# Kernel tuning notes

Hardware: AMD Instinct MI355X
Metric: run time of the kernel (lower is better)

Reference implementation:

```python
import jax, jax.numpy as jnp
import numpy as np

N = 100000      # nodes
E = 1600000     # edges
IN = 128        # in_channels
HID = 32        # hidden_channels
HEADS = 4
G = 256         # number of graphs in the batch
NEG_SLOPE = 0.2


def setup_inputs() -> dict:
    key = jax.random.key(0)
    ks = jax.random.split(key, 20)
    s = 0.1
    d = {
        'x': jax.random.normal(ks[0], (N, IN), jnp.float32),
        'edge_index': jax.random.randint(ks[1], (2, E), 0, N, dtype=jnp.int64),
        'batch': jnp.sort(jax.random.randint(ks[2], (N,), 0, G, dtype=jnp.int64)),
        # conv1: IN -> HID per head, HEADS heads, concat
        'W1': jax.random.normal(ks[3], (IN, HEADS * HID), jnp.float32) * s,
        'a_src1': jax.random.normal(ks[4], (HEADS, HID), jnp.float32) * s,
        'a_dst1': jax.random.normal(ks[5], (HEADS, HID), jnp.float32) * s,
        'b1': jnp.zeros((HEADS * HID,), jnp.float32),
        # conv2: HEADS*HID -> HID per head, HEADS heads, concat
        'W2': jax.random.normal(ks[6], (HEADS * HID, HEADS * HID), jnp.float32) * s,
        'a_src2': jax.random.normal(ks[7], (HEADS, HID), jnp.float32) * s,
        'a_dst2': jax.random.normal(ks[8], (HEADS, HID), jnp.float32) * s,
        'b2': jnp.zeros((HEADS * HID,), jnp.float32),
        # conv3: HEADS*HID -> HID, 1 head, no concat (mean over heads is identity)
        'W3': jax.random.normal(ks[9], (HEADS * HID, HID), jnp.float32) * s,
        'a_src3': jax.random.normal(ks[10], (1, HID), jnp.float32) * s,
        'a_dst3': jax.random.normal(ks[11], (1, HID), jnp.float32) * s,
        'b3': jnp.zeros((HID,), jnp.float32),
        # final readout
        'fc_w': jax.random.normal(ks[12], (HID, 1), jnp.float32) * s,
        'fc_b': jnp.zeros((1,), jnp.float32),
    }
    return d


def _gat_layer(x, src, dst, W, a_s, a_d, b, concat):
    """One PyG-style GATConv: edge attention logits, per-destination softmax, scatter-aggregate."""
    n = x.shape[0]
    H, C = a_s.shape
    h = (x @ W).reshape(n, H, C)                       # [N, H, C]
    asrc = (h * a_s).sum(-1)                           # [N, H]
    adst = (h * a_d).sum(-1)                           # [N, H]
    e = jax.nn.leaky_relu(asrc[src] + adst[dst], NEG_SLOPE)   # [Etot, H]
    m = jax.ops.segment_max(e, dst, num_segments=n)    # per-dst max (self-loops guarantee non-empty)
    ex = jnp.exp(e - m[dst])
    den = jax.ops.segment_sum(ex, dst, num_segments=n)
    alpha = ex / (den[dst] + 1e-16)                    # segment softmax, [Etot, H]
    out = jax.ops.segment_sum(alpha[:, :, None] * h[src], dst, num_segments=n)  # [N, H, C]
    if concat:
        return out.reshape(n, H * C) + b
    return out.mean(axis=1) + b


def reference(x, edge_index, batch, W1, a_src1, a_dst1, b1, W2, a_src2, a_dst2, b2,
              W3, a_src3, a_dst3, b3, fc_w, fc_b):
    n = x.shape[0]
    loops = jnp.arange(n, dtype=edge_index.dtype)      # GATConv adds self-loops by default
    src = jnp.concatenate([edge_index[0], loops])
    dst = jnp.concatenate([edge_index[1], loops])

    h = jax.nn.elu(_gat_layer(x, src, dst, W1, a_src1, a_dst1, b1, True))
    h = jax.nn.elu(_gat_layer(h, src, dst, W2, a_src2, a_dst2, b2, True))
    h = jax.nn.elu(_gat_layer(h, src, dst, W3, a_src3, a_dst3, b3, False))

    counts = jax.ops.segment_sum(jnp.ones((n,), h.dtype), batch, num_segments=G)
    pooled = jax.ops.segment_sum(h, batch, num_segments=G) / jnp.maximum(counts, 1.0)[:, None]
    # dropout p=0.5 is identity in eval mode
    return pooled @ fc_w + fc_b                        # [G, 1]
```

## Files before the change

### kernel.cpp

```cpp
#include <hip/hip_runtime.h>
#include <hip/hip_bf16.h>
#include <math.h>

#define NEG_SLOPE 0.2f
#define CHUNK 6144

typedef short bf16x8 __attribute__((ext_vector_type(8)));
typedef float f32x4  __attribute__((ext_vector_type(4)));

__device__ __forceinline__ float leaky(float x){ return x > 0.f ? x : NEG_SLOPE*x; }
__device__ __forceinline__ float elu(float x){ return x > 0.f ? x : expm1f(x); }

__device__ __forceinline__ ushort f2bf(float f){
  uint u = __float_as_uint(f);
  u += 0x7fffu + ((u >> 16) & 1u);
  return (ushort)(u >> 16);
}
__device__ __forceinline__ uint pk2(float lo, float hi){
  return (uint)f2bf(lo) | ((uint)f2bf(hi) << 16);
}
__device__ __forceinline__ float2 bfpair(uint v){
  return make_float2(__uint_as_float(v << 16), __uint_as_float(v & 0xffff0000u));
}

__global__ __launch_bounds__(256) void k_histA(const int* __restrict__ ei, int E,
                                               int* __restrict__ bucketCount){
  __shared__ int hist[512];
  for (int b = threadIdx.x; b < 512; b += 256) hist[b] = 0;
  __syncthreads();
  int base = blockIdx.x * 2048;
  int cnt = min(2048, E - base);
  for (int i = threadIdx.x; i < cnt; i += 256)
    atomicAdd(&hist[ei[E + base + i] >> 8], 1);
  __syncthreads();
  for (int b = threadIdx.x; b < 512; b += 256)
    if (hist[b]) atomicAdd(&bucketCount[b], hist[b]);
}

__global__ __launch_bounds__(256) void k_scanB(const int* __restrict__ bucketCount, int NB,
                        int* __restrict__ bucketBase, int* __restrict__ gcursor, int E){
  __shared__ int s[512];
  for (int b = threadIdx.x; b < 512; b += 256)
    s[b] = (b < NB) ? bucketCount[b] : 0;
  __syncthreads();
  if (threadIdx.x == 0){
    int run = 0;
    for (int b = 0; b < NB; b++){ int v = s[b]; s[b] = run; run += v; }
  }
  __syncthreads();
  for (int b = threadIdx.x; b < NB; b += 256){
    bucketBase[b] = s[b]; gcursor[b] = s[b];
  }
  if (threadIdx.x == 0) bucketBase[NB] = E;
}

__global__ __launch_bounds__(256) void k_scatA(const int* __restrict__ ei, int E, int NB,
                         int* __restrict__ gcursor, uint* __restrict__ tmp){
  __shared__ uint stageS[CHUNK];
  __shared__ uint stageD[CHUNK];
  __shared__ int hist[512], pre[512], cur[512], gbase[512];
  __shared__ int scanArr[256];
  int tid = threadIdx.x;
  int base = blockIdx.x * CHUNK;
  int cnt = min(CHUNK, E - base);
  for (int b = tid; b < 512; b += 256) hist[b] = 0;
  __syncthreads();
  for (int i = tid; i < cnt; i += 256)
    atomicAdd(&hist[ei[E + base + i] >> 8], 1);
  __syncthreads();
  int a0 = hist[2*tid], a1 = hist[2*tid+1];
  scanArr[tid] = a0 + a1;
  __syncthreads();
  for (int st = 1; st < 256; st <<= 1){
    int v = (tid >= st) ? scanArr[tid - st] : 0;
    __syncthreads();
    scanArr[tid] += v;
    __syncthreads();
  }
  int eb = tid ? scanArr[tid-1] : 0;
  pre[2*tid] = eb;        cur[2*tid] = eb;
  pre[2*tid+1] = eb + a0; cur[2*tid+1] = eb + a0;
  if (2*tid < NB && a0 > 0)   gbase[2*tid]   = atomicAdd(&gcursor[2*tid],   a0);
  if (2*tid+1 < NB && a1 > 0) gbase[2*tid+1] = atomicAdd(&gcursor[2*tid+1], a1);
  __syncthreads();
  for (int i = tid; i < cnt; i += 256){
    int s = ei[base + i];
    int d = ei[E + base + i];
    int lpos = atomicAdd(&cur[d >> 8], 1);
    stageS[lpos] = (uint)s; stageD[lpos] = (uint)d;
  }
  __syncthreads();
  for (int i = tid; i < cnt; i += 256){
    uint d = stageD[i];
    int b = d >> 8;
    tmp[gbase[b] + (i - pre[b])] = (stageS[i] << 8) | (d & 255u);
  }
}

__global__ __launch_bounds__(256) void k_csr(const uint* __restrict__ tmp,
                      const int* __restrict__ bucketBase,
                      int N, int NB, int* __restrict__ offsets, int* __restrict__ csr){
  int b = blockIdx.x;
  int nodeBase = b << 8;
  int nNodes = min(256, N - nodeBase);
  int eBeg = bucketBase[b], eEnd = bucketBase[b+1];
  __shared__ int deg[256], cur[256];
  int tid = threadIdx.x;
  deg[tid] = 0;
  __syncthreads();
  for (int e = eBeg + tid; e < eEnd; e += 256)
    atomicAdd(&deg[tmp[e] & 255u], 1);
  __syncthreads();
  cur[tid] = deg[tid];
  __syncthreads();
  for (int st = 1; st < 256; st <<= 1){
    int w = (tid >= st) ? cur[tid - st] : 0;
    __syncthreads();
    cur[tid] += w;
    __syncthreads();
  }
  int excl = tid ? cur[tid-1] : 0;
  __syncthreads();
  cur[tid] = excl;
  if (tid < nNodes) offsets[nodeBase + tid] = eBeg + excl;
  if (b == NB-1 && tid == 0) offsets[N] = eEnd;
  __syncthreads();
  for (int e = eBeg + tid; e < eEnd; e += 256){
    uint u = tmp[e];
    int lpos = atomicAdd(&cur[u & 255u], 1);
    csr[eBeg + lpos] = (int)(u >> 8);
  }
}

template<int NT>
__global__ __launch_bounds__(256) void k_wrep(const float* __restrict__ W, ushort* __restrict__ Wf){
  int idx = blockIdx.x*256 + threadIdx.x;
  if (idx >= NT*4*64) return;
  int lane = idx & 63;
  int c = (idx >> 6) & 3;
  int t = idx >> 8;
  int col = t*16 + (lane & 15);
  int k0 = c*32 + (lane >> 4)*8;
  uint4 o;
  const float* p0 = W + (size_t)k0*(NT*16) + col;
  o.x = pk2(p0[0],          p0[NT*16]);
  o.y = pk2(p0[2*NT*16],    p0[3*NT*16]);
  o.z = pk2(p0[4*NT*16],    p0[5*NT*16]);
  o.w = pk2(p0[6*NT*16],    p0[7*NT*16]);
  *(uint4*)(Wf + (size_t)idx*8) = o;
}

template<int NT, bool A_F32>
__global__ __launch_bounds__(256) void k_mgemm(const void* __restrict__ Xv,
                     const ushort* __restrict__ Wf, ushort* __restrict__ Y, int n){
  constexpr int M = NT*16;
  int lane = threadIdx.x & 63;
  int l15 = lane & 15, q = lane >> 4;
  int wgid = blockIdx.x*4 + (threadIdx.x >> 6);
  int nchunks = (n + 15) >> 4;
  int stride = gridDim.x*4;

  bf16x8 bw[NT][4];
  #pragma unroll
  for (int t = 0; t < NT; t++)
    #pragma unroll
    for (int c = 0; c < 4; c++)
      bw[t][c] = *(const bf16x8*)(Wf + (size_t)(((t<<2)+c)*64 + lane)*8);

  int chunk = wgid;
  if (chunk >= nchunks) return;

  bf16x8 aCur[4], aNext[4];
  auto loadA = [&](int ck, bf16x8* a){
    int m = ck*16 + l15;
    if (m >= n) m = n - 1;
    if (A_F32){
      const float* X = (const float*)Xv + (size_t)m*128 + q*8;
      #pragma unroll
      for (int c = 0; c < 4; c++){
        float4 u0 = *(const float4*)(X + c*32);
        float4 u1 = *(const float4*)(X + c*32 + 4);
        uint4 pkd;
        pkd.x = pk2(u0.x, u0.y); pkd.y = pk2(u0.z, u0.w);
        pkd.z = pk2(u1.x, u1.y); pkd.w = pk2(u1.z, u1.w);
        union { uint4 u; bf16x8 v; } cv; cv.u = pkd;
        a[c] = cv.v;
      }
    } else {
      const ushort* X = (const ushort*)Xv + (size_t)m*128 + q*8;
      #pragma unroll
      for (int c = 0; c < 4; c++) a[c] = *(const bf16x8*)(X + c*32);
    }
  };

  loadA(chunk, aCur);
  while (true){
    int nx = chunk + stride;
    if (nx < nchunks) loadA(nx, aNext);
    f32x4 acc[NT];
    #pragma unroll
    for (int t = 0; t < NT; t++) acc[t] = (f32x4){0.f,0.f,0.f,0.f};
    #pragma unroll
    for (int c = 0; c < 4; c++)
      #pragma unroll
      for (int t = 0; t < NT; t++)
        acc[t] = __builtin_amdgcn_mfma_f32_16x16x32_bf16(aCur[c], bw[t][c], acc[t], 0, 0, 0);
    int rowb = chunk*16 + q*4;
    #pragma unroll
    for (int t = 0; t < NT; t++)
      #pragma unroll
      for (int r = 0; r < 4; r++){
        int row = rowb + r;
        if (row < n) Y[(size_t)row*M + t*16 + l15] = f2bf(acc[t][r]);
      }
    if (nx >= nchunks) break;
    chunk = nx;
    #pragma unroll
    for (int c = 0; c < 4; c++) aCur[c] = aNext[c];
  }
}

__global__ __launch_bounds__(256) void k_attn(const ushort* __restrict__ Hb, const float* __restrict__ a_s,
                     const float* __restrict__ a_d, float* __restrict__ asrc, float* __restrict__ adst,
                     int n, int H, int M){
  int idx = blockIdx.x*256 + threadIdx.x;
  if (idx >= n*H) return;
  int node = idx / H, h = idx - node*H;
  const uint4* r4 = (const uint4*)(Hb + (size_t)node*M + h*32);
  const float* as = a_s + h*32;
  const float* ad = a_d + h*32;
  float s1 = 0.f, s2 = 0.f;
  #pragma unroll
  for (int i = 0; i < 4; i++){
    uint4 qv = r4[i];
    uint w[4] = {qv.x, qv.y, qv.z, qv.w};
    #pragma unroll
    for (int j = 0; j < 4; j++){
      float2 f = bfpair(w[j]);
      int c = i*8 + j*2;
      s1 += f.x*as[c] + f.y*as[c+1];
      s2 += f.x*ad[c] + f.y*ad[c+1];
    }
  }
  asrc[idx] = s1; adst[idx] = s2;
}

template<int HC, bool OUT_BF16>
__global__ __launch_bounds__(256) void k_agg(const ushort* __restrict__ Hb, const float* __restrict__ asrc,
                    const float* __restrict__ adst, const int* __restrict__ offsets,
                    const int* __restrict__ csr_src, const float* __restrict__ bias,
                    void* __restrict__ Out, int n){
  constexpr int H = HC/32;
  constexpr int PAIRS = HC/2;
  int gid = blockIdx.x*256 + threadIdx.x;
  int wave = gid >> 6;
  int lane = threadIdx.x & 63;
  int node, up;
  if (HC == 128){ node = wave;                 up = lane;      }
  else          { node = wave*4 + (lane >> 4); up = lane & 15; }
  if (node >= n) return;
  const int ch = up*2;
  const int h0 = ch >> 5;
  const uint* rows = (const uint*)Hb;
  float ad = adst[node*H + h0];
  float acc0 = 0.f, acc1 = 0.f, den = 0.f;
  {
    float w = __expf(leaky(asrc[node*H + h0] + ad));
    float2 f = bfpair(rows[(size_t)node*PAIRS + up]);
    den += w; acc0 += w*f.x; acc1 += w*f.y;
  }
  int j = offsets[node], end = offsets[node+1];
  for (; j + 4 <= end; j += 4){
    int s0 = csr_src[j], s1 = csr_src[j+1], s2 = csr_src[j+2], s3 = csr_src[j+3];
    if (HC == 128){
      s0 = __builtin_amdgcn_readfirstlane(s0);
      s1 = __builtin_amdgcn_readfirstlane(s1);
      s2 = __builtin_amdgcn_readfirstlane(s2);
      s3 = __builtin_amdgcn_readfirstlane(s3);
    }
    float e0 = asrc[s0*H + h0], e1 = asrc[s1*H + h0], e2 = asrc[s2*H + h0], e3 = asrc[s3*H + h0];
    uint r0 = rows[(size_t)s0*PAIRS + up];
    uint r1 = rows[(size_t)s1*PAIRS + up];
    uint r2 = rows[(size_t)s2*PAIRS + up];
    uint r3 = rows[(size_t)s3*PAIRS + up];
    float w0 = __expf(leaky(e0 + ad));
    float w1 = __expf(leaky(e1 + ad));
    float w2 = __expf(leaky(e2 + ad));
    float w3 = __expf(leaky(e3 + ad));
    float2 f0 = bfpair(r0), f1 = bfpair(r1), f2 = bfpair(r2), f3 = bfpair(r3);
    den  += (w0 + w1) + (w2 + w3);
    acc0 += w0*f0.x + w1*f1.x + w2*f2.x + w3*f3.x;
    acc1 += w0*f0.y + w1*f1.y + w2*f2.y + w3*f3.y;
  }
  for (; j < end; j++){
    int s = csr_src[j];
    if (HC == 128) s = __builtin_amdgcn_readfirstlane(s);
    float w = __expf(leaky(asrc[s*H + h0] + ad));
    float2 f = bfpair(rows[(size_t)s*PAIRS + up]);
    den += w; acc0 += w*f.x; acc1 += w*f.y;
  }
  float inv = 1.f/(den + 1e-16f);
  float ox = elu(acc0*inv + bias[ch]);
  float oy = elu(acc1*inv + bias[ch+1]);
  if (OUT_BF16){
    ((uint*)Out)[(size_t)node*PAIRS + up] = pk2(ox, oy);
  } else {
    *(float2*)((float*)Out + (size_t)node*HC + ch) = make_float2(ox, oy);
  }
}

__global__ __launch_bounds__(256) void k_bounds(const int* __restrict__ batch, int n, int G,
                                                int* __restrict__ gstart){
  int i = blockIdx.x*256 + threadIdx.x;
  if (i >= n) return;
  int b = batch[i];
  int bp = (i > 0) ? batch[i-1] : -1;
  for (int g = bp + 1; g <= b; g++) gstart[g] = i;
  if (i == n-1){
    for (int g = b + 1; g <= G; g++) gstart[g] = n;
  }
}

__global__ __launch_bounds__(256) void k_pool2(const float* __restrict__ H3,
                     const int* __restrict__ gstart, const float* __restrict__ fcw,
                     const float* __restrict__ fcb, float* __restrict__ out, int G){
  int g = blockIdx.x;
  int s0 = gstart[g], s1 = gstart[g+1];
  int tid = threadIdx.x;
  int c = tid & 31, r = tid >> 5;
  float sum = 0.f;
  for (int i = s0 + r; i < s1; i += 8)
    sum += H3[(size_t)i*32 + c];
  __shared__ float sh[8][32];
  sh[r][c] = sum;
  __syncthreads();
  if (tid < 32){
    float t = 0.f;
    #pragma unroll
    for (int k = 0; k < 8; k++) t += sh[k][tid];
    t *= fcw[tid];
    #pragma unroll
    for (int off = 16; off; off >>= 1) t += __shfl_down(t, off, 32);
    if (tid == 0){
      float cnt = (float)(s1 - s0); if (cnt < 1.f) cnt = 1.f;
      out[g] = t/cnt + fcb[0];
    }
  }
}

extern "C" void kernel_launch(void* const* d_in, const int* in_sizes, int n_in,
                              void* d_out, int out_size, void* d_ws, size_t ws_size,
                              hipStream_t stream){
  const float* x    = (const float*)d_in[0];
  const int*   ei   = (const int*)d_in[1];
  const int*   batch= (const int*)d_in[2];
  const float* W1   = (const float*)d_in[3];
  const float* as1  = (const float*)d_in[4];
  const float* ad1  = (const float*)d_in[5];
  const float* b1   = (const float*)d_in[6];
  const float* W2   = (const float*)d_in[7];
  const float* as2  = (const float*)d_in[8];
  const float* ad2  = (const float*)d_in[9];
  const float* b2   = (const float*)d_in[10];
  const float* W3   = (const float*)d_in[11];
  const float* as3  = (const float*)d_in[12];
  const float* ad3  = (const float*)d_in[13];
  const float* b3   = (const float*)d_in[14];
  const float* fcw  = (const float*)d_in[15];
  const float* fcb  = (const float*)d_in[16];
  float* out = (float*)d_out;

  const int N = in_sizes[0] / 128;
  const int E = in_sizes[1] / 2;
  const int G = out_size;
  const int NB = (N + 255) >> 8;

  char* p = (char*)d_ws;
  auto alloc = [&](size_t bytes) -> void* {
    void* r = (void*)p;
    p += (bytes + 255) & ~(size_t)255;
    return r;
  };
  ushort* bufH   = (ushort*)alloc((size_t)N*128*sizeof(ushort));
  ushort* aggB   = (ushort*)alloc((size_t)N*128*sizeof(ushort));
  float*  bufA32 = (float*)alloc((size_t)N*32*sizeof(float));
  float*  asrc   = (float*)alloc((size_t)N*4*sizeof(float));
  float*  adst   = (float*)alloc((size_t)N*4*sizeof(float));
  int*    offsets= (int*)alloc((size_t)(N+1)*sizeof(int));
  int*    csr    = (int*)alloc((size_t)E*sizeof(int));
  uint*   tmp    = (uint*)alloc((size_t)E*sizeof(uint));
  int*    bCount = (int*)alloc(512*sizeof(int));
  int*    bBase  = (int*)alloc(520*sizeof(int));
  int*    gcursor= (int*)alloc(512*sizeof(int));
  int*    gstart = (int*)alloc((size_t)(G+1)*sizeof(int));
  ushort* Wf1    = (ushort*)alloc(8*4*64*8*sizeof(ushort));
  ushort* Wf2    = (ushort*)alloc(8*4*64*8*sizeof(ushort));
  ushort* Wf3    = (ushort*)alloc(2*4*64*8*sizeof(ushort));

  hipMemsetAsync(bCount, 0, 512*sizeof(int), stream);

  k_wrep<8><<<8, 256, 0, stream>>>(W1, Wf1);
  k_wrep<8><<<8, 256, 0, stream>>>(W2, Wf2);
  k_wrep<2><<<2, 256, 0, stream>>>(W3, Wf3);

  k_histA<<<(E+2047)/2048, 256, 0, stream>>>(ei, E, bCount);
  k_scanB<<<1, 256, 0, stream>>>(bCount, NB, bBase, gcursor, E);
  k_scatA<<<(E+CHUNK-1)/CHUNK, 256, 0, stream>>>(ei, E, NB, gcursor, tmp);
  k_csr<<<NB, 256, 0, stream>>>(tmp, bBase, N, NB, offsets, csr);
  k_bounds<<<(N+255)/256, 256, 0, stream>>>(batch, N, G, gstart);

  const int GB = 512;
  k_mgemm<8, true ><<<GB, 256, 0, stream>>>(x, Wf1, bufH, N);
  k_attn<<<(N*4+255)/256, 256, 0, stream>>>(bufH, as1, ad1, asrc, adst, N, 4, 128);
  k_agg<128, true><<<(N*64+255)/256, 256, 0, stream>>>(bufH, asrc, adst, offsets, csr, b1, aggB, N);
  k_mgemm<8, false><<<GB, 256, 0, stream>>>(aggB, Wf2, bufH, N);
  k_attn<<<(N*4+255)/256, 256, 0, stream>>>(bufH, as2, ad2, asrc, adst, N, 4, 128);
  k_agg<128, true><<<(N*64+255)/256, 256, 0, stream>>>(bufH, asrc, adst, offsets, csr, b2, aggB, N);
  k_mgemm<2, false><<<GB, 256, 0, stream>>>(aggB, Wf3, bufH, N);
  k_attn<<<(N+255)/256, 256, 0, stream>>>(bufH, as3, ad3, asrc, adst, N, 1, 32);
  int waves3 = (N + 3)/4;
  k_agg<32, false><<<(waves3*64 + 255)/256, 256, 0, stream>>>(bufH, asrc, adst, offsets, csr, b3, bufA32, N);
  k_pool2<<<G, 256, 0, stream>>>(bufA32, gstart, fcw, fcb, out, G);
}
```

Measured before the change: 484.9 us.

## Precompute per-edge attention weights in a separate edge kernel before aggregation

Adds a destination index array in CSR order and a new per-edge kernel that computes exp(leaky(asrc[s]+adst[d])) for every edge and head, stored in an E×H buffer. The aggregation kernels then read these precomputed weights instead of gathering asrc and evaluating exp per lane. This removes redundant exp work and the scattered asrc gather inside aggregation. In exchange it adds three kernel launches, writes and reads an extra E×4 float buffer (about 25 MB per layer), and writes an extra edst array during CSR build.

After: 513.1 us. 1.06x slower.

```diff
diff --git a/kernel.cpp b/kernel.cpp
--- a/kernel.cpp
+++ b/kernel.cpp
@@ -99,7 +99,8 @@
 
 __global__ __launch_bounds__(256) void k_csr(const uint* __restrict__ tmp,
                       const int* __restrict__ bucketBase,
-                      int N, int NB, int* __restrict__ offsets, int* __restrict__ csr){
+                      int N, int NB, int* __restrict__ offsets, int* __restrict__ csr,
+                      int* __restrict__ edst){
   int b = blockIdx.x;
   int nodeBase = b << 8;
   int nNodes = min(256, N - nodeBase);
@@ -129,6 +130,7 @@
     uint u = tmp[e];
     int lpos = atomicAdd(&cur[u & 255u], 1);
     csr[eBeg + lpos] = (int)(u >> 8);
+    edst[eBeg + lpos] = nodeBase + (int)(u & 255u);
   }
 }
 
@@ -245,11 +247,33 @@
   asrc[idx] = s1; adst[idx] = s2;
 }
 
+template<int H>
+__global__ __launch_bounds__(256) void k_edgew(const float* __restrict__ asrc,
+                    const float* __restrict__ adst, const int* __restrict__ csr,
+                    const int* __restrict__ edst, float* __restrict__ ew, int E){
+  int e = blockIdx.x*256 + threadIdx.x;
+  if (e >= E) return;
+  int s = csr[e], d = edst[e];
+  if (H == 4){
+    float4 a = *(const float4*)(asrc + (size_t)s*4);
+    float4 b = *(const float4*)(adst + (size_t)d*4);
+    float4 w;
+    w.x = __expf(leaky(a.x + b.x));
+    w.y = __expf(leaky(a.y + b.y));
+    w.z = __expf(leaky(a.z + b.z));
+    w.w = __expf(leaky(a.w + b.w));
+    *(float4*)(ew + (size_t)e*4) = w;
+  } else {
+    ew[e] = __expf(leaky(asrc[s] + adst[d]));
+  }
+}
+
 template<int HC, bool OUT_BF16>
-__global__ __launch_bounds__(256) void k_agg(const ushort* __restrict__ Hb, const float* __restrict__ asrc,
-                    const float* __restrict__ adst, const int* __restrict__ offsets,
-                    const int* __restrict__ csr_src, const float* __restrict__ bias,
-                    void* __restrict__ Out, int n){
+__global__ __launch_bounds__(256) void k_agg(const ushort* __restrict__ Hb,
+                    const float* __restrict__ asrc, const float* __restrict__ adst,
+                    const float* __restrict__ ew,
+                    const int* __restrict__ offsets, const int* __restrict__ csr_src,
+                    const float* __restrict__ bias, void* __restrict__ Out, int n){
   constexpr int H = HC/32;
   constexpr int PAIRS = HC/2;
   int gid = blockIdx.x*256 + threadIdx.x;
@@ -262,10 +286,9 @@
   const int ch = up*2;
   const int h0 = ch >> 5;
   const uint* rows = (const uint*)Hb;
-  float ad = adst[node*H + h0];
   float acc0 = 0.f, acc1 = 0.f, den = 0.f;
   {
-    float w = __expf(leaky(asrc[node*H + h0] + ad));
+    float w = __expf(leaky(asrc[node*H + h0] + adst[node*H + h0]));
     float2 f = bfpair(rows[(size_t)node*PAIRS + up]);
     den += w; acc0 += w*f.x; acc1 += w*f.y;
   }
@@ -278,15 +301,14 @@
       s2 = __builtin_amdgcn_readfirstlane(s2);
       s3 = __builtin_amdgcn_readfirstlane(s3);
     }
-    float e0 = asrc[s0*H + h0], e1 = asrc[s1*H + h0], e2 = asrc[s2*H + h0], e3 = asrc[s3*H + h0];
+    float w0 = ew[(size_t)(j+0)*H + h0];
+    float w1 = ew[(size_t)(j+1)*H + h0];
+    float w2 = ew[(size_t)(j+2)*H + h0];
+    float w3 = ew[(size_t)(j+3)*H + h0];
     uint r0 = rows[(size_t)s0*PAIRS + up];
     uint r1 = rows[(size_t)s1*PAIRS + up];
     uint r2 = rows[(size_t)s2*PAIRS + up];
     uint r3 = rows[(size_t)s3*PAIRS + up];
-    float w0 = __expf(leaky(e0 + ad));
-    float w1 = __expf(leaky(e1 + ad));
-    float w2 = __expf(leaky(e2 + ad));
-    float w3 = __expf(leaky(e3 + ad));
     float2 f0 = bfpair(r0), f1 = bfpair(r1), f2 = bfpair(r2), f3 = bfpair(r3);
     den  += (w0 + w1) + (w2 + w3);
     acc0 += w0*f0.x + w1*f1.x + w2*f2.x + w3*f3.x;
@@ -295,7 +317,7 @@
   for (; j < end; j++){
     int s = csr_src[j];
     if (HC == 128) s = __builtin_amdgcn_readfirstlane(s);
-    float w = __expf(leaky(asrc[s*H + h0] + ad));
+    float w = ew[(size_t)j*H + h0];
     float2 f = bfpair(rows[(size_t)s*PAIRS + up]);
     den += w; acc0 += w*f.x; acc1 += w*f.y;
   }
@@ -386,8 +408,10 @@
   float*  bufA32 = (float*)alloc((size_t)N*32*sizeof(float));
   float*  asrc   = (float*)alloc((size_t)N*4*sizeof(float));
   float*  adst   = (float*)alloc((size_t)N*4*sizeof(float));
+  float*  ew     = (float*)alloc((size_t)E*4*sizeof(float));
   int*    offsets= (int*)alloc((size_t)(N+1)*sizeof(int));
   int*    csr    = (int*)alloc((size_t)E*sizeof(int));
+  int*    edst   = (int*)alloc((size_t)E*sizeof(int));
   uint*   tmp    = (uint*)alloc((size_t)E*sizeof(uint));
   int*    bCount = (int*)alloc(512*sizeof(int));
   int*    bBase  = (int*)alloc(520*sizeof(int));
@@ -406,19 +430,23 @@
   k_histA<<<(E+2047)/2048, 256, 0, stream>>>(ei, E, bCount);
   k_scanB<<<1, 256, 0, stream>>>(bCount, NB, bBase, gcursor, E);
   k_scatA<<<(E+CHUNK-1)/CHUNK, 256, 0, stream>>>(ei, E, NB, gcursor, tmp);
-  k_csr<<<NB, 256, 0, stream>>>(tmp, bBase, N, NB, offsets, csr);
+  k_csr<<<NB, 256, 0, stream>>>(tmp, bBase, N, NB, offsets, csr, edst);
   k_bounds<<<(N+255)/256, 256, 0, stream>>>(batch, N, G, gstart);
 
   const int GB = 512;
+  const int EBLK = (E+255)/256;
   k_mgemm<8, true ><<<GB, 256, 0, stream>>>(x, Wf1, bufH, N);
   k_attn<<<(N*4+255)/256, 256, 0, stream>>>(bufH, as1, ad1, asrc, adst, N, 4, 128);
-  k_agg<128, true><<<(N*64+255)/256, 256, 0, stream>>>(bufH, asrc, adst, offsets, csr, b1, aggB, N);
+  k_edgew<4><<<EBLK, 256, 0, stream>>>(asrc, adst, csr, edst, ew, E);
+  k_agg<128, true><<<(N*64+255)/256, 256, 0, stream>>>(bufH, asrc, adst, ew, offsets, csr, b1, aggB, N);
   k_mgemm<8, false><<<GB, 256, 0, stream>>>(aggB, Wf2, bufH, N);
   k_attn<<<(N*4+255)/256, 256, 0, stream>>>(bufH, as2, ad2, asrc, adst, N, 4, 128);
-  k_agg<128, true><<<(N*64+255)/256, 256, 0, stream>>>(bufH, asrc, adst, offsets, csr, b2, aggB, N);
+  k_edgew<4><<<EBLK, 256, 0, stream>>>(asrc, adst, csr, edst, ew, E);
+  k_agg<128, true><<<(N*64+255)/256, 256, 0, stream>>>(bufH, asrc, adst, ew, offsets, csr, b2, aggB, N);
   k_mgemm<2, false><<<GB, 256, 0, stream>>>(aggB, Wf3, bufH, N);
   k_attn<<<(N+255)/256, 256, 0, stream>>>(bufH, as3, ad3, asrc, adst, N, 1, 32);
+  k_edgew<1><<<EBLK, 256, 0, stream>>>(asrc, adst, csr, edst, ew, E);
   int waves3 = (N + 3)/4;
-  k_agg<32, false><<<(waves3*64 + 255)/256, 256, 0, stream>>>(bufH, asrc, adst, offsets, csr, b3, bufA32, N);
+  k_agg<32, false><<<(waves3*64 + 255)/256, 256, 0, stream>>>(bufH, asrc, adst, ew, offsets, csr, b3, bufA32, N);
   k_pool2<<<G, 256, 0, stream>>>(bufA32, gstart, fcw, fcb, out, G);
 }
```
